# Kernel optimization log

Hardware: AMD Instinct MI355X
Metric: run time of the kernel (lower is better)

Reference implementation:

```python
import jax, jax.numpy as jnp
import numpy as np

H = 1024      # hidden_size
NH = 16       # num_heads
HD = H // NH  # head_dim


def setup_inputs() -> dict:
    key = jax.random.key(0)
    ks = jax.random.split(key, 5)
    x = jax.random.normal(ks[0], (2, 2048, H), dtype=jnp.float32)
    # nn.Linear weights are [out, in]; keep that convention
    w_qkv = jax.random.normal(ks[1], (3 * H, H), dtype=jnp.float32) * (1.0 / np.sqrt(H))
    b_qkv = jax.random.normal(ks[2], (3 * H,), dtype=jnp.float32) * 0.01
    w_out = jax.random.normal(ks[3], (H, H), dtype=jnp.float32) * (1.0 / np.sqrt(H))
    b_out = jax.random.normal(ks[4], (H,), dtype=jnp.float32) * 0.01
    return {"x": x, "w_qkv": w_qkv, "b_qkv": b_qkv, "w_out": w_out, "b_out": b_out}


def reference(x, w_qkv, b_qkv, w_out, b_out):
    B, L, _ = x.shape
    scale = HD ** -0.5
    qkv = x @ w_qkv.T + b_qkv                       # [B,L,3H]
    qkv = qkv.reshape(B, L, 3, NH, HD).transpose(2, 0, 3, 1, 4)  # [3,B,NH,L,HD]
    q, k, v = qkv[0], qkv[1], qkv[2]
    attn = jnp.einsum('bhqd,bhkd->bhqk', q, k) * scale
    attn = jax.nn.softmax(attn, axis=-1)            # dropout is identity in eval
    out = jnp.einsum('bhqk,bhkd->bhqd', attn, v)    # [B,NH,L,HD]
    out = out.transpose(0, 2, 1, 3).reshape(B, L, H)
    return out @ w_out.T + b_out
```

## Files before the change

### kernel.cpp

```cpp
#include <hip/hip_runtime.h>
#include <hip/hip_bf16.h>
#include <stdint.h>

#define H_DIM  1024
#define NHEADS 16
#define HDIM   64
#define BATCH  2
#define SEQ    2048
#define MROWS  (BATCH * SEQ)
#define QKV_N  (3 * H_DIM)
#define QK_LD  (2 * H_DIM)
#define NT     (SEQ / 64)

typedef __attribute__((ext_vector_type(8))) __bf16 bf16x8;
typedef __attribute__((ext_vector_type(4))) float  floatx4;

__device__ __forceinline__ unsigned short f2bf(float f) {
    uint32_t u = __float_as_uint(f);
    u += 0x7fffu + ((u >> 16) & 1u);
    return (unsigned short)(u >> 16);
}
__device__ __forceinline__ float bf2f(unsigned short u) {
    return __uint_as_float(((uint32_t)u) << 16);
}
__device__ __forceinline__ uint32_t cvtpk_bf16(float lo, float hi) {
    uint32_t r;
    asm("v_cvt_pk_bf16_f32 %0, %1, %2" : "=v"(r) : "v"(lo), "v"(hi));
    return r;
}

__device__ __forceinline__ void async_ld16(const void* g, void* l) {
    __builtin_amdgcn_global_load_lds(
        (const __attribute__((address_space(1))) void*)g,
        (__attribute__((address_space(3))) void*)l, 16, 0, 0);
}

__global__ __launch_bounds__(256) void cvt_f32_bf16(const float4* __restrict__ in,
                                                    ushort4* __restrict__ out, int n4) {
    int i = blockIdx.x * 256 + threadIdx.x;
    if (i < n4) {
        float4 v = in[i];
        ushort4 o;
        o.x = f2bf(v.x); o.y = f2bf(v.y); o.z = f2bf(v.z); o.w = f2bf(v.w);
        out[i] = o;
    }
}

__global__ __launch_bounds__(256) void gemm_bt(const unsigned short* __restrict__ A,
                                               const unsigned short* __restrict__ B,
                                               const float* __restrict__ bias,
                                               unsigned short* __restrict__ Cb,
                                               float* __restrict__ Cf,
                                               unsigned short* __restrict__ Vt,
                                               int ldc, int Kdim) {
    __shared__ __align__(16) unsigned short As[128 * 32];
    __shared__ __align__(16) unsigned short Bs[128 * 32];
    const int tid  = threadIdx.x;
    const int lane = tid & 63;
    const int wave = tid >> 6;
    const int waveM = (wave >> 1) * 64;
    const int waveN = (wave & 1) * 64;
    const int bm = blockIdx.y, bn = blockIdx.x;

    floatx4 acc[4][4];
    #pragma unroll
    for (int i = 0; i < 4; ++i)
        #pragma unroll
        for (int j = 0; j < 4; ++j) {
            floatx4 z = {0.f, 0.f, 0.f, 0.f};
            acc[i][j] = z;
        }

    const int c0 = tid, c1 = tid + 256;
    const int r0 = c0 >> 2, kc0 = (c0 & 3) * 8;
    const int r1 = c1 >> 2, kc1 = (c1 & 3) * 8;
    char* asb0 = (char*)As + wave * 1024;
    char* asb1 = (char*)As + 4096 + wave * 1024;
    char* bsb0 = (char*)Bs + wave * 1024;
    char* bsb1 = (char*)Bs + 4096 + wave * 1024;

    const int lr = lane & 15;
    const int lk = (lane >> 4) * 8;

    for (int k0 = 0; k0 < Kdim; k0 += 32) {
        async_ld16(&A[(size_t)(bm * 128 + r0) * Kdim + k0 + kc0], asb0);
        async_ld16(&A[(size_t)(bm * 128 + r1) * Kdim + k0 + kc1], asb1);
        async_ld16(&B[(size_t)(bn * 128 + r0) * Kdim + k0 + kc0], bsb0);
        async_ld16(&B[(size_t)(bn * 128 + r1) * Kdim + k0 + kc1], bsb1);
        __syncthreads();

        bf16x8 af[4], bfr[4];
        #pragma unroll
        for (int i = 0; i < 4; ++i)
            af[i] = *(const bf16x8*)&As[(waveM + i * 16 + lr) * 32 + lk];
        #pragma unroll
        for (int j = 0; j < 4; ++j)
            bfr[j] = *(const bf16x8*)&Bs[(waveN + j * 16 + lr) * 32 + lk];

        #pragma unroll
        for (int i = 0; i < 4; ++i)
            #pragma unroll
            for (int j = 0; j < 4; ++j)
                acc[i][j] = __builtin_amdgcn_mfma_f32_16x16x32_bf16(af[i], bfr[j], acc[i][j], 0, 0, 0);
        __syncthreads();
    }

    const int crow0 = bm * 128 + waveM + (lane >> 4) * 4;
    const int ccol0 = bn * 128 + waveN + (lane & 15);
    #pragma unroll
    for (int i = 0; i < 4; ++i)
        #pragma unroll
        for (int j = 0; j < 4; ++j) {
            int col = ccol0 + j * 16;
            float bv = bias[col];
            #pragma unroll
            for (int r = 0; r < 4; ++r) {
                int row = crow0 + i * 16 + r;
                float v = acc[i][j][r] + bv;
                if (Vt && col >= 2 * H_DIM) {
                    int hd = col - 2 * H_DIM;
                    int bb = row >> 11, kv = row & (SEQ - 1);
                    int hh = hd >> 6,  dd = hd & 63;
                    Vt[((size_t)((bb << 4) + hh) * HDIM + dd) * SEQ + kv] = f2bf(v);
                } else if (Cb) {
                    Cb[(size_t)row * ldc + col] = f2bf(v);
                } else {
                    Cf[(size_t)row * ldc + col] = v;
                }
            }
        }
}

__global__ __launch_bounds__(256) void gemm_bt64(const unsigned short* __restrict__ A,
                                                 const unsigned short* __restrict__ B,
                                                 const float* __restrict__ bias,
                                                 float* __restrict__ Cf,
                                                 int ldc, int Kdim) {
    __shared__ __align__(16) unsigned short As[128 * 32];
    __shared__ __align__(16) unsigned short Bs[64 * 32];
    const int tid  = threadIdx.x;
    const int lane = tid & 63;
    const int wave = tid >> 6;
    const int waveM = wave * 32;
    const int bm = blockIdx.y, bn = blockIdx.x;

    floatx4 acc[2][4];
    #pragma unroll
    for (int i = 0; i < 2; ++i)
        #pragma unroll
        for (int j = 0; j < 4; ++j) {
            floatx4 z = {0.f, 0.f, 0.f, 0.f};
            acc[i][j] = z;
        }

    const int c0 = tid, c1 = tid + 256;
    const int r0 = c0 >> 2, kc0 = (c0 & 3) * 8;
    const int r1 = c1 >> 2, kc1 = (c1 & 3) * 8;
    char* asb0 = (char*)As + wave * 1024;
    char* asb1 = (char*)As + 4096 + wave * 1024;
    char* bsb0 = (char*)Bs + wave * 1024;

    const int lr = lane & 15;
    const int lk = (lane >> 4) * 8;

    for (int k0 = 0; k0 < Kdim; k0 += 32) {
        async_ld16(&A[(size_t)(bm * 128 + r0) * Kdim + k0 + kc0], asb0);
        async_ld16(&A[(size_t)(bm * 128 + r1) * Kdim + k0 + kc1], asb1);
        async_ld16(&B[(size_t)(bn * 64 + r0) * Kdim + k0 + kc0], bsb0);
        __syncthreads();

        bf16x8 af[2], bfr[4];
        #pragma unroll
        for (int i = 0; i < 2; ++i)
            af[i] = *(const bf16x8*)&As[(waveM + i * 16 + lr) * 32 + lk];
        #pragma unroll
        for (int j = 0; j < 4; ++j)
            bfr[j] = *(const bf16x8*)&Bs[(j * 16 + lr) * 32 + lk];

        #pragma unroll
        for (int i = 0; i < 2; ++i)
            #pragma unroll
            for (int j = 0; j < 4; ++j)
                acc[i][j] = __builtin_amdgcn_mfma_f32_16x16x32_bf16(af[i], bfr[j], acc[i][j], 0, 0, 0);
        __syncthreads();
    }

    const int crow0 = bm * 128 + waveM + (lane >> 4) * 4;
    const int ccol0 = bn * 64 + (lane & 15);
    #pragma unroll
    for (int i = 0; i < 2; ++i)
        #pragma unroll
        for (int j = 0; j < 4; ++j) {
            int col = ccol0 + j * 16;
            float bv = bias[col];
            #pragma unroll
            for (int r = 0; r < 4; ++r) {
                int row = crow0 + i * 16 + r;
                Cf[(size_t)row * ldc + col] = acc[i][j][r] + bv;
            }
        }
}

__global__ __launch_bounds__(256, 4) void attn_mfma(const unsigned short* __restrict__ qkv2,
                                                    const unsigned short* __restrict__ vt,
                                                    unsigned short* __restrict__ ctx) {
    __shared__ __align__(16) unsigned short Ks2[2][64 * 64];
    __shared__ __align__(16) unsigned short Vt2[2][64 * 64];
    __shared__ __align__(16) unsigned short Ps [4][16 * 64];

    const int tid  = threadIdx.x;
    const int lane = tid & 63;
    const int wave = tid >> 6;
    const int bh = blockIdx.y;
    const int b  = bh >> 4, h = bh & 15;
    const int q0 = blockIdx.x * 64 + wave * 16;
    const int lq = lane & 15;
    const int g  = lane >> 4;
    const int swz = lq & 7;

    unsigned short* Pw = &Ps[wave][0];

    const float QS = 0.125f * 1.44269504f;
    bf16x8 qf[2];
    #pragma unroll
    for (int kk = 0; kk < 2; ++kk) {
        union { bf16x8 v; unsigned short u[8]; } tq;
        tq.v = *(const bf16x8*)&qkv2[(size_t)(b * SEQ + q0 + lq) * QK_LD
                                     + h * HDIM + kk * 32 + g * 8];
        #pragma unroll
        for (int e = 0; e < 8; ++e) tq.u[e] = f2bf(bf2f(tq.u[e]) * QS);
        qf[kk] = tq.v;
    }

    floatx4 acc_o[4];
    #pragma unroll
    for (int j = 0; j < 4; ++j) {
        floatx4 z = {0.f, 0.f, 0.f, 0.f};
        acc_o[j] = z;
    }
    float l_run = 0.f;

    const unsigned short* gK = qkv2 + (size_t)b * SEQ * QK_LD + H_DIM + (size_t)h * HDIM;
    const unsigned short* gV = vt + (size_t)bh * HDIM * SEQ;

    const int r0 = tid >> 3,         gs0 = (tid & 7) ^ (r0 & 7);
    const int r1 = (256 + tid) >> 3, gs1 = ((256 + tid) & 7) ^ (r1 & 7);
    const unsigned short* pK0 = gK + (size_t)r0 * QK_LD + gs0 * 8;
    const unsigned short* pK1 = gK + (size_t)r1 * QK_LD + gs1 * 8;
    const unsigned short* pV0 = gV + (size_t)r0 * SEQ + gs0 * 8;
    const unsigned short* pV1 = gV + (size_t)r1 * SEQ + gs1 * 8;

    #define STAGE_KV(bi)                                                        \
        {                                                                       \
            async_ld16(pK0, (char*)&Ks2[bi][0] + (wave * 64) * 16);             \
            async_ld16(pK1, (char*)&Ks2[bi][0] + (256 + wave * 64) * 16);       \
            async_ld16(pV0, (char*)&Vt2[bi][0] + (wave * 64) * 16);             \
            async_ld16(pV1, (char*)&Vt2[bi][0] + (256 + wave * 64) * 16);       \
            pK0 += 64 * QK_LD; pK1 += 64 * QK_LD; pV0 += 64; pV1 += 64;         \
        }

    STAGE_KV(0)
    __syncthreads();

    int buf = 0;
    for (int t = 0; t < NT; ++t) {
        if (t + 1 < NT) STAGE_KV(buf ^ 1)

        const unsigned short* Ksb = &Ks2[buf][0];
        const unsigned short* Vsb = &Vt2[buf][0];

        bf16x8 kf[4][2];
        #pragma unroll
        for (int jb = 0; jb < 4; ++jb)
            #pragma unroll
            for (int kk = 0; kk < 2; ++kk)
                kf[jb][kk] = *(const bf16x8*)&Ksb[(jb * 16 + lq) * 64 + (((kk << 2) + g) ^ swz) * 8];

        bf16x8 vf[4][2];
        #pragma unroll
        for (int dt = 0; dt < 4; ++dt)
            #pragma unroll
            for (int kk = 0; kk < 2; ++kk)
                vf[dt][kk] = *(const bf16x8*)&Vsb[(dt * 16 + lq) * 64 + (((kk << 2) + g) ^ swz) * 8];

        __builtin_amdgcn_sched_barrier(0);

        floatx4 sa[4];
        #pragma unroll
        for (int jb = 0; jb < 4; ++jb) {
            floatx4 z = {0.f, 0.f, 0.f, 0.f};
            sa[jb] = z;
        }
        __builtin_amdgcn_s_setprio(1);
        #pragma unroll
        for (int jb = 0; jb < 4; ++jb)
            #pragma unroll
            for (int kk = 0; kk < 2; ++kk)
                sa[jb] = __builtin_amdgcn_mfma_f32_16x16x32_bf16(kf[jb][kk], qf[kk], sa[jb], 0, 0, 0);
        __builtin_amdgcn_s_setprio(0);

        float ps = 0.f;
        #pragma unroll
        for (int jb = 0; jb < 2; ++jb) {
            float p0 = exp2f(sa[jb][0]), p1 = exp2f(sa[jb][1]);
            float p2 = exp2f(sa[jb][2]), p3 = exp2f(sa[jb][3]);
            ps += (p0 + p1) + (p2 + p3);
            uint2 pk;
            pk.x = cvtpk_bf16(p0, p1);
            pk.y = cvtpk_bf16(p2, p3);
            *(uint2*)&Pw[lq * 64 + ((jb * 16 + g * 4) ^ (swz << 3))] = pk;
        }
        bf16x8 pf0 = *(const bf16x8*)&Pw[lq * 64 + ((g * 8) ^ (swz << 3))];
        __builtin_amdgcn_s_setprio(1);
        #pragma unroll
        for (int dt = 0; dt < 4; ++dt)
            acc_o[dt] = __builtin_amdgcn_mfma_f32_16x16x32_bf16(pf0, vf[dt][0], acc_o[dt], 0, 0, 0);
        __builtin_amdgcn_s_setprio(0);

        #pragma unroll
        for (int jb = 2; jb < 4; ++jb) {
            float p0 = exp2f(sa[jb][0]), p1 = exp2f(sa[jb][1]);
            float p2 = exp2f(sa[jb][2]), p3 = exp2f(sa[jb][3]);
            ps += (p0 + p1) + (p2 + p3);
            uint2 pk;
            pk.x = cvtpk_bf16(p0, p1);
            pk.y = cvtpk_bf16(p2, p3);
            *(uint2*)&Pw[lq * 64 + ((jb * 16 + g * 4) ^ (swz << 3))] = pk;
        }
        bf16x8 pf1 = *(const bf16x8*)&Pw[lq * 64 + ((32 + g * 8) ^ (swz << 3))];
        __builtin_amdgcn_s_setprio(1);
        #pragma unroll
        for (int dt = 0; dt < 4; ++dt)
            acc_o[dt] = __builtin_amdgcn_mfma_f32_16x16x32_bf16(pf1, vf[dt][1], acc_o[dt], 0, 0, 0);
        __builtin_amdgcn_s_setprio(0);

        ps += __shfl_xor(ps, 16);
        ps += __shfl_xor(ps, 32);
        l_run += ps;

        __syncthreads();
        buf ^= 1;
    }
    #undef STAGE_KV

    float linv[4];
    #pragma unroll
    for (int r = 0; r < 4; ++r)
        linv[r] = 1.f / __shfl(l_run, g * 4 + r);
    #pragma unroll
    for (int dt = 0; dt < 4; ++dt)
        #pragma unroll
        for (int r = 0; r < 4; ++r)
            ctx[(size_t)(b * SEQ + q0 + g * 4 + r) * H_DIM + h * HDIM + dt * 16 + lq]
                = f2bf(acc_o[dt][r] * linv[r]);
}

extern "C" void kernel_launch(void* const* d_in, const int* in_sizes, int n_in,
                              void* d_out, int out_size, void* d_ws, size_t ws_size,
                              hipStream_t stream) {
    const float* x     = (const float*)d_in[0];
    const float* w_qkv = (const float*)d_in[1];
    const float* b_qkv = (const float*)d_in[2];
    const float* w_out = (const float*)d_in[3];
    const float* b_out = (const float*)d_in[4];
    float* out = (float*)d_out;

    unsigned short* xb    = (unsigned short*)d_ws;
    unsigned short* wqkvb = xb    + (size_t)MROWS * H_DIM;
    unsigned short* woutb = wqkvb + (size_t)QKV_N * H_DIM;
    unsigned short* qkv2  = woutb + (size_t)H_DIM * H_DIM;
    unsigned short* ctxb  = qkv2  + (size_t)MROWS * QK_LD;
    unsigned short* vtb   = ctxb  + (size_t)MROWS * H_DIM;

    cvt_f32_bf16<<<MROWS * H_DIM / 1024, 256, 0, stream>>>((const float4*)x,     (ushort4*)xb,    MROWS * H_DIM / 4);
    cvt_f32_bf16<<<QKV_N * H_DIM / 1024, 256, 0, stream>>>((const float4*)w_qkv, (ushort4*)wqkvb, QKV_N * H_DIM / 4);
    cvt_f32_bf16<<<H_DIM * H_DIM / 1024, 256, 0, stream>>>((const float4*)w_out, (ushort4*)woutb, H_DIM * H_DIM / 4);

    gemm_bt<<<dim3(QKV_N / 128, MROWS / 128), 256, 0, stream>>>(xb, wqkvb, b_qkv, qkv2, nullptr, vtb, QK_LD, H_DIM);

    attn_mfma<<<dim3(SEQ / 64, BATCH * NHEADS), 256, 0, stream>>>(qkv2, vtb, ctxb);

    gemm_bt64<<<dim3(H_DIM / 64, MROWS / 128), 256, 0, stream>>>(ctxb, woutb, b_out, out, H_DIM, H_DIM);
}
```

Before: 219.1 us.

## Permute K rows at load to feed P directly from registers, drop LDS roundtrip

K rows are loaded into shared memory in a permuted order, so the S accumulator layout from the QK^T MFMA already matches the A-operand layout needed for the PV MFMA. The per-wave P scratch in LDS, with its write-then-read roundtrip, is removed and P is packed to bf16 straight from registers. This cuts LDS traffic and latency on the critical path and frees shared memory. Correctness depends on the row permutation exactly matching the MFMA register layouts.

```diff
diff --git a/kernel.cpp b/kernel.cpp
--- a/kernel.cpp
+++ b/kernel.cpp
@@ -206,7 +206,6 @@
                                                     unsigned short* __restrict__ ctx) {
     __shared__ __align__(16) unsigned short Ks2[2][64 * 64];
     __shared__ __align__(16) unsigned short Vt2[2][64 * 64];
-    __shared__ __align__(16) unsigned short Ps [4][16 * 64];
 
     const int tid  = threadIdx.x;
     const int lane = tid & 63;
@@ -218,8 +217,6 @@
     const int g  = lane >> 4;
     const int swz = lq & 7;
 
-    unsigned short* Pw = &Ps[wave][0];
-
     const float QS = 0.125f * 1.44269504f;
     bf16x8 qf[2];
     #pragma unroll
@@ -243,12 +240,13 @@
     const unsigned short* gK = qkv2 + (size_t)b * SEQ * QK_LD + H_DIM + (size_t)h * HDIM;
     const unsigned short* gV = vt + (size_t)bh * HDIM * SEQ;
 
-    const int r0 = tid >> 3,         gs0 = (tid & 7) ^ (r0 & 7);
-    const int r1 = (256 + tid) >> 3, gs1 = ((256 + tid) & 7) ^ (r1 & 7);
-    const unsigned short* pK0 = gK + (size_t)r0 * QK_LD + gs0 * 8;
-    const unsigned short* pK1 = gK + (size_t)r1 * QK_LD + gs1 * 8;
+    const int r0  = tid >> 3;
+    const int pr0 = (r0 & 32) | ((r0 & 12) << 1) | ((r0 & 16) >> 2) | (r0 & 3);
+    const int gs0 = (tid & 7) ^ (r0 & 7);
+    const unsigned short* pK0 = gK + (size_t)pr0 * QK_LD + gs0 * 8;
+    const unsigned short* pK1 = gK + (size_t)(pr0 + 32) * QK_LD + gs0 * 8;
     const unsigned short* pV0 = gV + (size_t)r0 * SEQ + gs0 * 8;
-    const unsigned short* pV1 = gV + (size_t)r1 * SEQ + gs1 * 8;
+    const unsigned short* pV1 = gV + (size_t)(r0 + 32) * SEQ + gs0 * 8;
 
     #define STAGE_KV(bi)                                                        \
         {                                                                       \
@@ -300,39 +298,34 @@
         __builtin_amdgcn_s_setprio(0);
 
         float ps = 0.f;
-        #pragma unroll
-        for (int jb = 0; jb < 2; ++jb) {
-            float p0 = exp2f(sa[jb][0]), p1 = exp2f(sa[jb][1]);
-            float p2 = exp2f(sa[jb][2]), p3 = exp2f(sa[jb][3]);
-            ps += (p0 + p1) + (p2 + p3);
-            uint2 pk;
-            pk.x = cvtpk_bf16(p0, p1);
-            pk.y = cvtpk_bf16(p2, p3);
-            *(uint2*)&Pw[lq * 64 + ((jb * 16 + g * 4) ^ (swz << 3))] = pk;
-        }
-        bf16x8 pf0 = *(const bf16x8*)&Pw[lq * 64 + ((g * 8) ^ (swz << 3))];
-        __builtin_amdgcn_s_setprio(1);
-        #pragma unroll
-        for (int dt = 0; dt < 4; ++dt)
-            acc_o[dt] = __builtin_amdgcn_mfma_f32_16x16x32_bf16(pf0, vf[dt][0], acc_o[dt], 0, 0, 0);
-        __builtin_amdgcn_s_setprio(0);
-
-        #pragma unroll
-        for (int jb = 2; jb < 4; ++jb) {
-            float p0 = exp2f(sa[jb][0]), p1 = exp2f(sa[jb][1]);
-            float p2 = exp2f(sa[jb][2]), p3 = exp2f(sa[jb][3]);
-            ps += (p0 + p1) + (p2 + p3);
-            uint2 pk;
-            pk.x = cvtpk_bf16(p0, p1);
-            pk.y = cvtpk_bf16(p2, p3);
-            *(uint2*)&Pw[lq * 64 + ((jb * 16 + g * 4) ^ (swz << 3))] = pk;
-        }
-        bf16x8 pf1 = *(const bf16x8*)&Pw[lq * 64 + ((32 + g * 8) ^ (swz << 3))];
-        __builtin_amdgcn_s_setprio(1);
-        #pragma unroll
-        for (int dt = 0; dt < 4; ++dt)
-            acc_o[dt] = __builtin_amdgcn_mfma_f32_16x16x32_bf16(pf1, vf[dt][1], acc_o[dt], 0, 0, 0);
-        __builtin_amdgcn_s_setprio(0);
+
+        {
+            float e00 = exp2f(sa[0][0]), e01 = exp2f(sa[0][1]), e02 = exp2f(sa[0][2]), e03 = exp2f(sa[0][3]);
+            float e10 = exp2f(sa[1][0]), e11 = exp2f(sa[1][1]), e12 = exp2f(sa[1][2]), e13 = exp2f(sa[1][3]);
+            ps += ((e00 + e01) + (e02 + e03)) + ((e10 + e11) + (e12 + e13));
+            union { bf16x8 v; uint32_t u[4]; } pf;
+            pf.u[0] = cvtpk_bf16(e00, e01); pf.u[1] = cvtpk_bf16(e02, e03);
+            pf.u[2] = cvtpk_bf16(e10, e11); pf.u[3] = cvtpk_bf16(e12, e13);
+            __builtin_amdgcn_s_setprio(1);
+            #pragma unroll
+            for (int dt = 0; dt < 4; ++dt)
+                acc_o[dt] = __builtin_amdgcn_mfma_f32_16x16x32_bf16(pf.v, vf[dt][0], acc_o[dt], 0, 0, 0);
+            __builtin_amdgcn_s_setprio(0);
+        }
+
+        {
+            float e00 = exp2f(sa[2][0]), e01 = exp2f(sa[2][1]), e02 = exp2f(sa[2][2]), e03 = exp2f(sa[2][3]);
+            float e10 = exp2f(sa[3][0]), e11 = exp2f(sa[3][1]), e12 = exp2f(sa[3][2]), e13 = exp2f(sa[3][3]);
+            ps += ((e00 + e01) + (e02 + e03)) + ((e10 + e11) + (e12 + e13));
+            union { bf16x8 v; uint32_t u[4]; } pf;
+            pf.u[0] = cvtpk_bf16(e00, e01); pf.u[1] = cvtpk_bf16(e02, e03);
+            pf.u[2] = cvtpk_bf16(e10, e11); pf.u[3] = cvtpk_bf16(e12, e13);
+            __builtin_amdgcn_s_setprio(1);
+            #pragma unroll
+            for (int dt = 0; dt < 4; ++dt)
+                acc_o[dt] = __builtin_amdgcn_mfma_f32_16x16x32_bf16(pf.v, vf[dt][1], acc_o[dt], 0, 0, 0);
+            __builtin_amdgcn_s_setprio(0);
+        }
 
         ps += __shfl_xor(ps, 16);
         ps += __shfl_xor(ps, 32);
```

Result: no change. 219.0 us (-0.1%).
